# Kernel optimization log

Hardware: AMD Instinct MI355X
Metric: run time of the kernel (lower is better)

The kernel has to match this reference:

```python
import jax, jax.numpy as jnp
import numpy as np

B, N, DIM, H, DH = 2, 2048, 512, 8, 64
EPS = 1e-3  # eps added after relu feature map, per original


def setup_inputs() -> dict:
    key = jax.random.key(0)
    k0, k1, k2, k3, k4 = jax.random.split(key, 5)
    s_in = 1.0 / np.sqrt(DIM)
    s_out = 1.0 / np.sqrt(H * DH)
    return {
        "x": jax.random.normal(k0, (B, N, DIM), jnp.float32),
        "Wq": jax.random.normal(k1, (DIM, H * DH), jnp.float32) * s_in,
        "Wk": jax.random.normal(k2, (DIM, H * DH), jnp.float32) * s_in,
        "Wv": jax.random.normal(k3, (DIM, H * DH), jnp.float32) * s_in,
        "Wo": jax.random.normal(k4, (H * DH, DIM), jnp.float32) * s_out,
        "bo": jnp.zeros((DIM,), jnp.float32),
    }


def causal_linear_attn(q, k, v, eps=EPS):
    # bucket_size == 1 path of the original causal_linear_attn (blindspot_size=1):
    # relu feature map + eps, running cumsums of k and of the outer product k v^T.
    q = jax.nn.relu(q) + eps
    k = jax.nn.relu(k) + eps
    k_cum = jnp.cumsum(k, axis=2)                                  # [b,h,n,d]
    ctx = jnp.cumsum(k[..., :, None] * v[..., None, :], axis=2)    # [b,h,n,d,e]
    d_inv = 1.0 / jnp.einsum('bhnd,bhnd->bhn', q, k_cum)           # [b,h,n]
    return jnp.einsum('bhnd,bhnde,bhn->bhne', q, ctx, d_inv)       # [b,h,n,e]


def reference(x, Wq, Wk, Wv, Wo, bo):
    b, n, _ = x.shape
    split = lambda t: t.reshape(b, n, H, DH).transpose(0, 2, 1, 3)  # [b,h,n,dh]
    q = split(x @ Wq)
    k = split(x @ Wk)
    v = split(x @ Wv)
    out = causal_linear_attn(q, k, v)
    out = out.transpose(0, 2, 1, 3).reshape(b, n, H * DH)
    return out @ Wo + bo
```

## Files before the change

### kernel.cpp

```cpp
#include <hip/hip_runtime.h>

constexpr int kB   = 2;
constexpr int kN   = 2048;
constexpr int kDIM = 512;
constexpr int kH   = 8;
constexpr int kDH  = 64;
constexpr int kBH  = kB * kH;
constexpr int NROWS = kB * kN;
constexpr int CHUNK = 64;
constexpr int NCH   = kN / CHUNK;
constexpr int CBSTRIDE = kDH * kDH + kDH;
constexpr float kEPS = 1e-3f;

typedef _Float16 f16x8 __attribute__((ext_vector_type(8)));
typedef _Float16 f16x4 __attribute__((ext_vector_type(4)));
typedef float    floatx4 __attribute__((ext_vector_type(4)));

__device__ __forceinline__ void async_copy16(void* lds, const void* g) {
    __builtin_amdgcn_global_load_lds(
        (const __attribute__((address_space(1))) void*)g,
        (__attribute__((address_space(3))) void*)lds,
        16, 0, 0);
}

__global__ __launch_bounds__(256)
void convert_x_kernel(const float* __restrict__ x, _Float16* __restrict__ xh)
{
    const int i = blockIdx.x * 256 + threadIdx.x;
    const float4 a = *(const float4*)(x + (size_t)i * 8);
    const float4 b = *(const float4*)(x + (size_t)i * 8 + 4);
    f16x8 o;
    o[0] = (_Float16)a.x; o[1] = (_Float16)a.y; o[2] = (_Float16)a.z; o[3] = (_Float16)a.w;
    o[4] = (_Float16)b.x; o[5] = (_Float16)b.y; o[6] = (_Float16)b.z; o[7] = (_Float16)b.w;
    *(f16x8*)(xh + (size_t)i * 8) = o;
}

__global__ __launch_bounds__(256)
void convert_wT_kernel(const float* __restrict__ Wq, const float* __restrict__ Wk,
                       const float* __restrict__ Wv, const float* __restrict__ Wo,
                       _Float16* __restrict__ WT, _Float16* __restrict__ WoT)
{
    __shared__ float tile[32][33];
    const int z = blockIdx.z;
    const float* src = (z == 0) ? Wq : (z == 1) ? Wk : (z == 2) ? Wv : Wo;
    _Float16* dst = (z < 3) ? (WT + (size_t)z * 512 * 512) : WoT;
    const int r0 = blockIdx.y * 32, c0 = blockIdx.x * 32;
    const int tr = threadIdx.x >> 5, tc = threadIdx.x & 31;
    #pragma unroll
    for (int i = 0; i < 4; ++i)
        tile[tr + 8 * i][tc] = src[(size_t)(r0 + tr + 8 * i) * 512 + c0 + tc];
    __syncthreads();
    #pragma unroll
    for (int i = 0; i < 4; ++i)
        dst[(size_t)(c0 + tr + 8 * i) * 512 + r0 + tc] = (_Float16)tile[tc][tr + 8 * i];
}

template<int MODE>
__global__ __launch_bounds__(256)
void mfma_gemm_kernel(const _Float16* __restrict__ A,
                      const _Float16* __restrict__ BT,
                      const float* __restrict__ bo,
                      float* __restrict__ o0,
                      float* __restrict__ o1,
                      float* __restrict__ o2)
{
    constexpr int BM = 128, BN = 128, BK = 64, K = 512;
    __shared__ _Float16 As[BM * BK];
    __shared__ _Float16 Bs[BN * BK];

    const int t = threadIdx.x;
    const int l = t & 63;
    const int w = t >> 6;
    const int wm = w >> 1, wn = w & 1;
    const int m0 = blockIdx.x * BM;
    const int n0 = blockIdx.y * BN;

    const int r15 = l & 15, kq = l >> 4, sw = r15 & 7;

    floatx4 acc[4][4];
    #pragma unroll
    for (int mi = 0; mi < 4; ++mi)
        #pragma unroll
        for (int ni = 0; ni < 4; ++ni)
            acc[mi][ni] = (floatx4){0.f, 0.f, 0.f, 0.f};

    const int srow  = t >> 3;
    const int sslot = t & 7;

    const char* Abase = (const char*)(A + (size_t)m0 * K);
    const char* Bbase = (const char*)(BT + (size_t)n0 * K);
    char* AsB = (char*)As;
    char* BsB = (char*)Bs;

    const char* ArdB = (const char*)As + (wm * 64 + r15) * 128;
    const char* BrdB = (const char*)Bs + (wn * 64 + r15) * 128;
    const int sw0 = ((kq ^ sw) << 4);
    const int sw1 = (((4 + kq) ^ sw) << 4);

    for (int k0 = 0; k0 < K; k0 += BK) {
        #pragma unroll
        for (int i = 0; i < 4; ++i) {
            const int row = i * 32 + srow;
            const int gsl = sslot ^ (row & 7);
            async_copy16(AsB + row * 128 + sslot * 16,
                         Abase + (size_t)row * (K * 2) + k0 * 2 + gsl * 16);
            async_copy16(BsB + row * 128 + sslot * 16,
                         Bbase + (size_t)row * (K * 2) + k0 * 2 + gsl * 16);
        }
        __syncthreads();

        f16x8 af[4][2], bf[4][2];
        #pragma unroll
        for (int i = 0; i < 4; ++i) {
            af[i][0] = *(const f16x8*)(ArdB + i * 2048 + sw0);
            af[i][1] = *(const f16x8*)(ArdB + i * 2048 + sw1);
            bf[i][0] = *(const f16x8*)(BrdB + i * 2048 + sw0);
            bf[i][1] = *(const f16x8*)(BrdB + i * 2048 + sw1);
        }
        #pragma unroll
        for (int kh = 0; kh < 2; ++kh)
            #pragma unroll
            for (int mi = 0; mi < 4; ++mi)
                #pragma unroll
                for (int ni = 0; ni < 4; ++ni)
                    acc[mi][ni] = __builtin_amdgcn_mfma_f32_16x16x32_f16(
                        af[mi][kh], bf[ni][kh], acc[mi][ni], 0, 0, 0);
        __syncthreads();
    }

    if (MODE == 0) {
        const int which = n0 >> 9;
        float* dst = (which == 0) ? o0 : (which == 1) ? o1 : o2;
        #pragma unroll
        for (int ni = 0; ni < 4; ++ni) {
            const int col = n0 + wn * 64 + ni * 16 + r15;
            const int h = (col >> 6) & 7, e = col & 63;
            #pragma unroll
            for (int mi = 0; mi < 4; ++mi) {
                #pragma unroll
                for (int r = 0; r < 4; ++r) {
                    const int row = m0 + wm * 64 + mi * 16 + kq * 4 + r;
                    const int b = row >> 11, n = row & 2047;
                    float v = acc[mi][ni][r];
                    if (which < 2) v = fmaxf(v, 0.f) + kEPS;
                    dst[((size_t)((b << 3) + h) * 2048 + n) * 64 + e] = v;
                }
            }
        }
    } else {
        #pragma unroll
        for (int ni = 0; ni < 4; ++ni) {
            const int col = n0 + wn * 64 + ni * 16 + r15;
            const float bias = bo[col];
            #pragma unroll
            for (int mi = 0; mi < 4; ++mi) {
                const int row = m0 + wm * 64 + mi * 16 + kq * 4;
                #pragma unroll
                for (int r = 0; r < 4; ++r)
                    o0[(size_t)(row + r) * 512 + col] = acc[mi][ni][r] + bias;
            }
        }
    }
}

__global__ __launch_bounds__(256)
void chunk_sum_kernel(const float* __restrict__ kb, const float* __restrict__ vb,
                      float* __restrict__ cbuf)
{
    const int ch = blockIdx.x, bh = blockIdx.y;
    const int t = threadIdx.x;
    const int tx = t & 15, ty = t >> 4;

    __shared__ float ks[64][65];
    __shared__ float vs[64][68];

    const float* kp = kb + ((size_t)bh * kN + (size_t)ch * CHUNK) * kDH;
    const float* vp = vb + ((size_t)bh * kN + (size_t)ch * CHUNK) * kDH;

    #pragma unroll
    for (int it = 0; it < 4; ++it) {
        int idx = it * 1024 + t * 4;
        int row = idx >> 6, col = idx & 63;
        float4 k4 = *(const float4*)(kp + (size_t)row * kDH + col);
        ks[row][col + 0] = k4.x; ks[row][col + 1] = k4.y;
        ks[row][col + 2] = k4.z; ks[row][col + 3] = k4.w;
        float4 v4 = *(const float4*)(vp + (size_t)row * kDH + col);
        vs[row][col + 0] = v4.x; vs[row][col + 1] = v4.y;
        vs[row][col + 2] = v4.z; vs[row][col + 3] = v4.w;
    }
    __syncthreads();

    float acc[4][4] = {};
    for (int n = 0; n < 64; ++n) {
        float kr[4], vr[4];
        #pragma unroll
        for (int i = 0; i < 4; ++i) kr[i] = ks[n][ty * 4 + i];
        #pragma unroll
        for (int j = 0; j < 4; ++j) vr[j] = vs[n][tx * 4 + j];
        #pragma unroll
        for (int i = 0; i < 4; ++i)
            #pragma unroll
            for (int j = 0; j < 4; ++j)
                acc[i][j] += kr[i] * vr[j];
    }

    float* out = cbuf + ((size_t)bh * NCH + ch) * CBSTRIDE;
    #pragma unroll
    for (int i = 0; i < 4; ++i) {
        float4 o; o.x = acc[i][0]; o.y = acc[i][1]; o.z = acc[i][2]; o.w = acc[i][3];
        *(float4*)(out + (size_t)(ty * 4 + i) * kDH + tx * 4) = o;
    }
    if (t < 64) {
        float z = 0.f;
        for (int n = 0; n < 64; ++n) z += ks[n][t];
        out[kDH * kDH + t] = z;
    }
}

__global__ __launch_bounds__(256)
void prefix_kernel(float* __restrict__ cbuf)
{
    const int bh = blockIdx.y;
    const int i = blockIdx.x * 256 + threadIdx.x;
    if (i >= CBSTRIDE) return;
    float* base = cbuf + (size_t)bh * NCH * CBSTRIDE + i;
    float vals[NCH];
    #pragma unroll
    for (int c = 0; c < NCH; ++c) vals[c] = base[(size_t)c * CBSTRIDE];
    float acc = 0.f;
    #pragma unroll
    for (int c = 0; c < NCH; ++c) {
        float tmp = vals[c];
        base[(size_t)c * CBSTRIDE] = acc;
        acc += tmp;
    }
}

__global__ __launch_bounds__(256)
void chunk_out_kernel(const float* __restrict__ qb, const float* __restrict__ kb,
                      const float* __restrict__ vb, const float* __restrict__ cbuf,
                      _Float16* __restrict__ attnh)
{
    const int ch = blockIdx.x, bh = blockIdx.y;
    const int t = threadIdx.x;
    const int tx = t & 15, ty = t >> 4;

    __shared__ float qs[64][65];
    __shared__ float kvs[64][68];
    __shared__ float asA[64][65];
    __shared__ float denp[64][17];
    __shared__ float denf[64];

    const float* qp = qb + ((size_t)bh * kN + (size_t)ch * CHUNK) * kDH;
    const float* kp = kb + ((size_t)bh * kN + (size_t)ch * CHUNK) * kDH;
    const float* vp = vb + ((size_t)bh * kN + (size_t)ch * CHUNK) * kDH;
    const float* spre = cbuf + ((size_t)bh * NCH + ch) * CBSTRIDE;

    #pragma unroll
    for (int it = 0; it < 4; ++it) {
        int idx = it * 1024 + t * 4;
        int row = idx >> 6, col = idx & 63;
        float4 q4 = *(const float4*)(qp + (size_t)row * kDH + col);
        qs[row][col + 0] = q4.x; qs[row][col + 1] = q4.y;
        qs[row][col + 2] = q4.z; qs[row][col + 3] = q4.w;
        float4 k4 = *(const float4*)(kp + (size_t)row * kDH + col);
        kvs[row][col + 0] = k4.x; kvs[row][col + 1] = k4.y;
        kvs[row][col + 2] = k4.z; kvs[row][col + 3] = k4.w;
    }
    __syncthreads();

    float acc[4][4] = {};
    for (int d = 0; d < 64; ++d) {
        float qr[4], kr[4];
        #pragma unroll
        for (int i = 0; i < 4; ++i) qr[i] = qs[ty * 4 + i][d];
        #pragma unroll
        for (int j = 0; j < 4; ++j) kr[j] = kvs[tx * 4 + j][d];
        #pragma unroll
        for (int i = 0; i < 4; ++i)
            #pragma unroll
            for (int j = 0; j < 4; ++j)
                acc[i][j] += qr[i] * kr[j];
    }
    __syncthreads();

    #pragma unroll
    for (int i = 0; i < 4; ++i) {
        float p = 0.f;
        #pragma unroll
        for (int j = 0; j < 4; ++j) {
            float a = (tx * 4 + j <= ty * 4 + i) ? acc[i][j] : 0.f;
            asA[ty * 4 + i][tx * 4 + j] = a;
            p += a;
        }
        denp[ty * 4 + i][tx] = p;
    }
    #pragma unroll
    for (int it = 0; it < 4; ++it) {
        int idx = it * 1024 + t * 4;
        int row = idx >> 6, col = idx & 63;
        float4 v4 = *(const float4*)(vp + (size_t)row * kDH + col);
        kvs[row][col + 0] = v4.x; kvs[row][col + 1] = v4.y;
        kvs[row][col + 2] = v4.z; kvs[row][col + 3] = v4.w;
    }
    __syncthreads();

    if (t < 64) {
        float dsum = 0.f;
        #pragma unroll
        for (int x2 = 0; x2 < 16; ++x2) dsum += denp[t][x2];
        const float* z = spre + kDH * kDH;
        for (int d = 0; d < 64; ++d) dsum += qs[t][d] * z[d];
        denf[t] = 1.0f / dsum;
    }

    float o[4][4] = {};
    for (int m = 0; m < 64; ++m) {
        float ar[4], vr[4];
        #pragma unroll
        for (int i = 0; i < 4; ++i) ar[i] = asA[ty * 4 + i][m];
        #pragma unroll
        for (int j = 0; j < 4; ++j) vr[j] = kvs[m][tx * 4 + j];
        #pragma unroll
        for (int i = 0; i < 4; ++i)
            #pragma unroll
            for (int j = 0; j < 4; ++j)
                o[i][j] += ar[i] * vr[j];
    }
    for (int d = 0; d < 64; ++d) {
        float qr[4];
        #pragma unroll
        for (int i = 0; i < 4; ++i) qr[i] = qs[ty * 4 + i][d];
        const float4 s4 = *(const float4*)(spre + (size_t)d * kDH + tx * 4);
        #pragma unroll
        for (int i = 0; i < 4; ++i) {
            o[i][0] += qr[i] * s4.x; o[i][1] += qr[i] * s4.y;
            o[i][2] += qr[i] * s4.z; o[i][3] += qr[i] * s4.w;
        }
    }
    __syncthreads();

    const int b = bh >> 3, h = bh & 7;
    #pragma unroll
    for (int i = 0; i < 4; ++i) {
        int n = ch * CHUNK + ty * 4 + i;
        float di = denf[ty * 4 + i];
        f16x4 st;
        st[0] = (_Float16)(o[i][0] * di);
        st[1] = (_Float16)(o[i][1] * di);
        st[2] = (_Float16)(o[i][2] * di);
        st[3] = (_Float16)(o[i][3] * di);
        *(f16x4*)(attnh + (((size_t)(b * kN + n)) << 9) + h * 64 + tx * 4) = st;
    }
}

extern "C" void kernel_launch(void* const* d_in, const int* in_sizes, int n_in,
                              void* d_out, int out_size, void* d_ws, size_t ws_size,
                              hipStream_t stream)
{
    const float* x  = (const float*)d_in[0];
    const float* Wq = (const float*)d_in[1];
    const float* Wk = (const float*)d_in[2];
    const float* Wv = (const float*)d_in[3];
    const float* Wo = (const float*)d_in[4];
    const float* bo = (const float*)d_in[5];
    float* out = (float*)d_out;

    char* ws = (char*)d_ws;
    float*    qb    = (float*)(ws + 0);
    float*    kb    = (float*)(ws + 8388608);
    float*    vb    = (float*)(ws + 16777216);
    float*    cbuf  = (float*)(ws + 25165824);
    _Float16* xh    = (_Float16*)(ws + 33685504);
    _Float16* WT    = (_Float16*)(ws + 37879808);
    _Float16* WoT   = (_Float16*)(ws + 39452672);
    _Float16* attnh = xh;

    convert_x_kernel<<<1024, 256, 0, stream>>>(x, xh);
    convert_wT_kernel<<<dim3(16, 16, 4), 256, 0, stream>>>(Wq, Wk, Wv, Wo, WT, WoT);
    mfma_gemm_kernel<0><<<dim3(NROWS / 128, 12), 256, 0, stream>>>(xh, WT, nullptr, qb, kb, vb);
    chunk_sum_kernel<<<dim3(NCH, kBH), 256, 0, stream>>>(kb, vb, cbuf);
    prefix_kernel<<<dim3(17, kBH), 256, 0, stream>>>(cbuf);
    chunk_out_kernel<<<dim3(NCH, kBH), 256, 0, stream>>>(qb, kb, vb, cbuf, attnh);
    mfma_gemm_kernel<1><<<dim3(NROWS / 128, 4), 256, 0, stream>>>(attnh, WoT, bo, out, nullptr, nullptr);
}
```

Measured before the change: 68.23 us.

## Move chunked linear-attention math to fp16 MFMA with transposed K/V layouts

The QKV projection now writes q, k and v as fp16, plus transposed copies of k and v, in place of fp32 buffers. The chunk-sum and chunk-output kernels replace scalar FMA loops with 16x16x32 fp16 MFMA instructions, and the prefix scan emits an fp16 copy of the state together with an fp32 normaliser. This should cut memory traffic and scalar ALU work in the attention stages, at the cost of extra transposed writes and reduced precision in the intermediates.

```diff
diff --git a/kernel.cpp b/kernel.cpp
--- a/kernel.cpp
+++ b/kernel.cpp
@@ -60,9 +60,11 @@
 void mfma_gemm_kernel(const _Float16* __restrict__ A,
                       const _Float16* __restrict__ BT,
                       const float* __restrict__ bo,
-                      float* __restrict__ o0,
-                      float* __restrict__ o1,
-                      float* __restrict__ o2)
+                      float* __restrict__ outf,
+                      _Float16* __restrict__ qh,
+                      _Float16* __restrict__ khb,
+                      _Float16* __restrict__ kTh,
+                      _Float16* __restrict__ vTh)
 {
     constexpr int BM = 128, BN = 128, BK = 64, K = 512;
     __shared__ _Float16 As[BM * BK];
@@ -118,32 +120,51 @@
             bf[i][1] = *(const f16x8*)(BrdB + i * 2048 + sw1);
         }
         #pragma unroll
-        for (int kh = 0; kh < 2; ++kh)
+        for (int kk = 0; kk < 2; ++kk)
             #pragma unroll
             for (int mi = 0; mi < 4; ++mi)
                 #pragma unroll
                 for (int ni = 0; ni < 4; ++ni)
                     acc[mi][ni] = __builtin_amdgcn_mfma_f32_16x16x32_f16(
-                        af[mi][kh], bf[ni][kh], acc[mi][ni], 0, 0, 0);
+                        af[mi][kk], bf[ni][kk], acc[mi][ni], 0, 0, 0);
         __syncthreads();
     }
 
     if (MODE == 0) {
-        const int which = n0 >> 9;
-        float* dst = (which == 0) ? o0 : (which == 1) ? o1 : o2;
         #pragma unroll
         for (int ni = 0; ni < 4; ++ni) {
             const int col = n0 + wn * 64 + ni * 16 + r15;
+            const int which = col >> 9;
             const int h = (col >> 6) & 7, e = col & 63;
             #pragma unroll
             for (int mi = 0; mi < 4; ++mi) {
+                const int row0 = m0 + wm * 64 + mi * 16 + kq * 4;
+                const int b = row0 >> 11, nn = row0 & 2047;
+                const int bh = b * 8 + h;
+                float vv[4];
                 #pragma unroll
                 for (int r = 0; r < 4; ++r) {
-                    const int row = m0 + wm * 64 + mi * 16 + kq * 4 + r;
-                    const int b = row >> 11, n = row & 2047;
                     float v = acc[mi][ni][r];
                     if (which < 2) v = fmaxf(v, 0.f) + kEPS;
-                    dst[((size_t)((b << 3) + h) * 2048 + n) * 64 + e] = v;
+                    vv[r] = v;
+                }
+                if (which == 0) {
+                    #pragma unroll
+                    for (int r = 0; r < 4; ++r)
+                        qh[((size_t)bh * kN + nn + r) * 64 + e] = (_Float16)vv[r];
+                } else if (which == 1) {
+                    #pragma unroll
+                    for (int r = 0; r < 4; ++r)
+                        khb[((size_t)bh * kN + nn + r) * 64 + e] = (_Float16)vv[r];
+                    f16x4 t4;
+                    t4[0] = (_Float16)vv[0]; t4[1] = (_Float16)vv[1];
+                    t4[2] = (_Float16)vv[2]; t4[3] = (_Float16)vv[3];
+                    *(f16x4*)(kTh + ((size_t)bh * 64 + e) * kN + nn) = t4;
+                } else {
+                    f16x4 t4;
+                    t4[0] = (_Float16)vv[0]; t4[1] = (_Float16)vv[1];
+                    t4[2] = (_Float16)vv[2]; t4[3] = (_Float16)vv[3];
+                    *(f16x4*)(vTh + ((size_t)bh * 64 + e) * kN + nn) = t4;
                 }
             }
         }
@@ -157,200 +178,197 @@
                 const int row = m0 + wm * 64 + mi * 16 + kq * 4;
                 #pragma unroll
                 for (int r = 0; r < 4; ++r)
-                    o0[(size_t)(row + r) * 512 + col] = acc[mi][ni][r] + bias;
+                    outf[(size_t)(row + r) * 512 + col] = acc[mi][ni][r] + bias;
             }
         }
     }
 }
 
 __global__ __launch_bounds__(256)
-void chunk_sum_kernel(const float* __restrict__ kb, const float* __restrict__ vb,
+void chunk_sum_kernel(const _Float16* __restrict__ kTh, const _Float16* __restrict__ vTh,
                       float* __restrict__ cbuf)
 {
     const int ch = blockIdx.x, bh = blockIdx.y;
-    const int t = threadIdx.x;
-    const int tx = t & 15, ty = t >> 4;
-
-    __shared__ float ks[64][65];
-    __shared__ float vs[64][68];
-
-    const float* kp = kb + ((size_t)bh * kN + (size_t)ch * CHUNK) * kDH;
-    const float* vp = vb + ((size_t)bh * kN + (size_t)ch * CHUNK) * kDH;
-
-    #pragma unroll
-    for (int it = 0; it < 4; ++it) {
-        int idx = it * 1024 + t * 4;
-        int row = idx >> 6, col = idx & 63;
-        float4 k4 = *(const float4*)(kp + (size_t)row * kDH + col);
-        ks[row][col + 0] = k4.x; ks[row][col + 1] = k4.y;
-        ks[row][col + 2] = k4.z; ks[row][col + 3] = k4.w;
-        float4 v4 = *(const float4*)(vp + (size_t)row * kDH + col);
-        vs[row][col + 0] = v4.x; vs[row][col + 1] = v4.y;
-        vs[row][col + 2] = v4.z; vs[row][col + 3] = v4.w;
-    }
-    __syncthreads();
-
-    float acc[4][4] = {};
-    for (int n = 0; n < 64; ++n) {
-        float kr[4], vr[4];
-        #pragma unroll
-        for (int i = 0; i < 4; ++i) kr[i] = ks[n][ty * 4 + i];
-        #pragma unroll
-        for (int j = 0; j < 4; ++j) vr[j] = vs[n][tx * 4 + j];
-        #pragma unroll
-        for (int i = 0; i < 4; ++i)
+    const int t = threadIdx.x, l = t & 63, w = t >> 6;
+    const int r15 = l & 15, kq = l >> 4;
+
+    const _Float16* vbase = vTh + (size_t)bh * 64 * kN + ch * 64;
+    const _Float16* kbase = kTh + (size_t)bh * 64 * kN + ch * 64;
+
+    f16x8 av[2], bk[4][2];
+    #pragma unroll
+    for (int kk = 0; kk < 2; ++kk) {
+        av[kk] = *(const f16x8*)(vbase + (size_t)(w * 16 + r15) * kN + kk * 32 + kq * 8);
+        #pragma unroll
+        for (int ni = 0; ni < 4; ++ni)
+            bk[ni][kk] = *(const f16x8*)(kbase + (size_t)(ni * 16 + r15) * kN + kk * 32 + kq * 8);
+    }
+    floatx4 acc[4];
+    #pragma unroll
+    for (int ni = 0; ni < 4; ++ni) acc[ni] = (floatx4){0.f, 0.f, 0.f, 0.f};
+    #pragma unroll
+    for (int kk = 0; kk < 2; ++kk)
+        #pragma unroll
+        for (int ni = 0; ni < 4; ++ni)
+            acc[ni] = __builtin_amdgcn_mfma_f32_16x16x32_f16(av[kk], bk[ni][kk], acc[ni], 0, 0, 0);
+
+    float* out = cbuf + ((size_t)bh * NCH + ch) * CBSTRIDE;
+    #pragma unroll
+    for (int ni = 0; ni < 4; ++ni)
+        #pragma unroll
+        for (int r = 0; r < 4; ++r)
+            out[(size_t)(w * 16 + kq * 4 + r) * 64 + ni * 16 + r15] = acc[ni][r];
+
+    if (t < 64) {
+        const _Float16* kp = kbase + (size_t)t * kN;
+        float z = 0.f;
+        #pragma unroll
+        for (int j = 0; j < 8; ++j) {
+            f16x8 v8 = *(const f16x8*)(kp + j * 8);
             #pragma unroll
-            for (int j = 0; j < 4; ++j)
-                acc[i][j] += kr[i] * vr[j];
-    }
-
-    float* out = cbuf + ((size_t)bh * NCH + ch) * CBSTRIDE;
-    #pragma unroll
-    for (int i = 0; i < 4; ++i) {
-        float4 o; o.x = acc[i][0]; o.y = acc[i][1]; o.z = acc[i][2]; o.w = acc[i][3];
-        *(float4*)(out + (size_t)(ty * 4 + i) * kDH + tx * 4) = o;
-    }
-    if (t < 64) {
-        float z = 0.f;
-        for (int n = 0; n < 64; ++n) z += ks[n][t];
-        out[kDH * kDH + t] = z;
-    }
-}
-
-__global__ __launch_bounds__(256)
-void prefix_kernel(float* __restrict__ cbuf)
+            for (int u = 0; u < 8; ++u) z += (float)v8[u];
+        }
+        out[4096 + t] = z;
+    }
+}
+
+__global__ __launch_bounds__(256)
+void prefix_kernel(const float* __restrict__ cbuf, _Float16* __restrict__ spre16,
+                   float* __restrict__ zpre)
 {
     const int bh = blockIdx.y;
     const int i = blockIdx.x * 256 + threadIdx.x;
     if (i >= CBSTRIDE) return;
-    float* base = cbuf + (size_t)bh * NCH * CBSTRIDE + i;
+    const float* src = cbuf + (size_t)bh * NCH * CBSTRIDE + i;
+    _Float16* dst = spre16 + (size_t)bh * NCH * CBSTRIDE + i;
+    float* zp = zpre + (size_t)bh * NCH * 64;
+    const bool isz = (i >= 4096);
     float vals[NCH];
     #pragma unroll
-    for (int c = 0; c < NCH; ++c) vals[c] = base[(size_t)c * CBSTRIDE];
-    float acc = 0.f;
+    for (int c = 0; c < NCH; ++c) vals[c] = src[(size_t)c * CBSTRIDE];
+    float a = 0.f;
     #pragma unroll
     for (int c = 0; c < NCH; ++c) {
-        float tmp = vals[c];
-        base[(size_t)c * CBSTRIDE] = acc;
-        acc += tmp;
-    }
-}
-
-__global__ __launch_bounds__(256)
-void chunk_out_kernel(const float* __restrict__ qb, const float* __restrict__ kb,
-                      const float* __restrict__ vb, const float* __restrict__ cbuf,
-                      _Float16* __restrict__ attnh)
+        dst[(size_t)c * CBSTRIDE] = (_Float16)a;
+        if (isz) zp[c * 64 + (i - 4096)] = a;
+        a += vals[c];
+    }
+}
+
+__global__ __launch_bounds__(256)
+void chunk_out_kernel(const _Float16* __restrict__ qh, const _Float16* __restrict__ khb,
+                      const _Float16* __restrict__ vTh, const _Float16* __restrict__ spre16,
+                      const float* __restrict__ zpre, _Float16* __restrict__ attnh)
 {
     const int ch = blockIdx.x, bh = blockIdx.y;
-    const int t = threadIdx.x;
-    const int tx = t & 15, ty = t >> 4;
-
-    __shared__ float qs[64][65];
-    __shared__ float kvs[64][68];
-    __shared__ float asA[64][65];
-    __shared__ float denp[64][17];
+    const int t = threadIdx.x, l = t & 63, w = t >> 6;
+    const int r15 = l & 15, kq = l >> 4;
+
+    __shared__ _Float16 Plds[64 * 64];
+    __shared__ float denp[64];
     __shared__ float denf[64];
 
-    const float* qp = qb + ((size_t)bh * kN + (size_t)ch * CHUNK) * kDH;
-    const float* kp = kb + ((size_t)bh * kN + (size_t)ch * CHUNK) * kDH;
-    const float* vp = vb + ((size_t)bh * kN + (size_t)ch * CHUNK) * kDH;
-    const float* spre = cbuf + ((size_t)bh * NCH + ch) * CBSTRIDE;
-
-    #pragma unroll
-    for (int it = 0; it < 4; ++it) {
-        int idx = it * 1024 + t * 4;
-        int row = idx >> 6, col = idx & 63;
-        float4 q4 = *(const float4*)(qp + (size_t)row * kDH + col);
-        qs[row][col + 0] = q4.x; qs[row][col + 1] = q4.y;
-        qs[row][col + 2] = q4.z; qs[row][col + 3] = q4.w;
-        float4 k4 = *(const float4*)(kp + (size_t)row * kDH + col);
-        kvs[row][col + 0] = k4.x; kvs[row][col + 1] = k4.y;
-        kvs[row][col + 2] = k4.z; kvs[row][col + 3] = k4.w;
+    const size_t rowbase = (size_t)bh * kN + ch * 64;
+
+    f16x8 aq[2], bk[4][2];
+    #pragma unroll
+    for (int kk = 0; kk < 2; ++kk) {
+        aq[kk] = *(const f16x8*)(qh + (rowbase + w * 16 + r15) * 64 + kk * 32 + kq * 8);
+        #pragma unroll
+        for (int ni = 0; ni < 4; ++ni)
+            bk[ni][kk] = *(const f16x8*)(khb + (rowbase + ni * 16 + r15) * 64 + kk * 32 + kq * 8);
+    }
+    floatx4 sacc[4];
+    #pragma unroll
+    for (int ni = 0; ni < 4; ++ni) sacc[ni] = (floatx4){0.f, 0.f, 0.f, 0.f};
+    #pragma unroll
+    for (int kk = 0; kk < 2; ++kk)
+        #pragma unroll
+        for (int ni = 0; ni < 4; ++ni)
+            sacc[ni] = __builtin_amdgcn_mfma_f32_16x16x32_f16(aq[kk], bk[ni][kk], sacc[ni], 0, 0, 0);
+
+    const int qrow = w * 16 + kq * 4;
+    float psum[4] = {0.f, 0.f, 0.f, 0.f};
+    #pragma unroll
+    for (int ni = 0; ni < 4; ++ni) {
+        const int m = ni * 16 + r15;
+        #pragma unroll
+        for (int r = 0; r < 4; ++r) {
+            const int row = qrow + r;
+            const float v = (m <= row) ? sacc[ni][r] : 0.f;
+            psum[r] += v;
+            const int byte = row * 128 + ((((unsigned)m >> 3) ^ (row & 7)) << 4) + (m & 7) * 2;
+            *(_Float16*)((char*)Plds + byte) = (_Float16)v;
+        }
+    }
+    #pragma unroll
+    for (int r = 0; r < 4; ++r) {
+        float p = psum[r];
+        p += __shfl_xor(p, 1, 16);
+        p += __shfl_xor(p, 2, 16);
+        p += __shfl_xor(p, 4, 16);
+        p += __shfl_xor(p, 8, 16);
+        if (r15 == 0) denp[qrow + r] = p;
     }
     __syncthreads();
 
-    float acc[4][4] = {};
-    for (int d = 0; d < 64; ++d) {
-        float qr[4], kr[4];
-        #pragma unroll
-        for (int i = 0; i < 4; ++i) qr[i] = qs[ty * 4 + i][d];
-        #pragma unroll
-        for (int j = 0; j < 4; ++j) kr[j] = kvs[tx * 4 + j][d];
-        #pragma unroll
-        for (int i = 0; i < 4; ++i)
+    if (t < 64) {
+        const _Float16* qp = qh + (rowbase + t) * 64;
+        const float* zp = zpre + ((size_t)bh * NCH + ch) * 64;
+        float s = denp[t];
+        #pragma unroll
+        for (int j = 0; j < 8; ++j) {
+            f16x8 q8 = *(const f16x8*)(qp + j * 8);
             #pragma unroll
-            for (int j = 0; j < 4; ++j)
-                acc[i][j] += qr[i] * kr[j];
-    }
+            for (int u = 0; u < 8; ++u) s += (float)q8[u] * zp[j * 8 + u];
+        }
+        denf[t] = 1.0f / s;
+    }
+
+    f16x8 ap[2], bv[4][2], bs[4][2];
+    #pragma unroll
+    for (int km = 0; km < 2; ++km)
+        ap[km] = *(const f16x8*)((char*)Plds + (w * 16 + r15) * 128 +
+                                 (((km * 4 + kq) ^ (r15 & 7)) << 4));
+    #pragma unroll
+    for (int ni = 0; ni < 4; ++ni) {
+        #pragma unroll
+        for (int km = 0; km < 2; ++km)
+            bv[ni][km] = *(const f16x8*)(vTh + ((size_t)bh * 64 + ni * 16 + r15) * kN +
+                                         ch * 64 + km * 32 + kq * 8);
+    }
+    const _Float16* sp = spre16 + ((size_t)bh * NCH + ch) * CBSTRIDE;
+    #pragma unroll
+    for (int ni = 0; ni < 4; ++ni)
+        #pragma unroll
+        for (int kd = 0; kd < 2; ++kd)
+            bs[ni][kd] = *(const f16x8*)(sp + (size_t)(ni * 16 + r15) * 64 + kd * 32 + kq * 8);
+
+    floatx4 oacc[4];
+    #pragma unroll
+    for (int ni = 0; ni < 4; ++ni) oacc[ni] = (floatx4){0.f, 0.f, 0.f, 0.f};
+    #pragma unroll
+    for (int km = 0; km < 2; ++km)
+        #pragma unroll
+        for (int ni = 0; ni < 4; ++ni)
+            oacc[ni] = __builtin_amdgcn_mfma_f32_16x16x32_f16(ap[km], bv[ni][km], oacc[ni], 0, 0, 0);
+    #pragma unroll
+    for (int kd = 0; kd < 2; ++kd)
+        #pragma unroll
+        for (int ni = 0; ni < 4; ++ni)
+            oacc[ni] = __builtin_amdgcn_mfma_f32_16x16x32_f16(aq[kd], bs[ni][kd], oacc[ni], 0, 0, 0);
     __syncthreads();
 
-    #pragma unroll
-    for (int i = 0; i < 4; ++i) {
-        float p = 0.f;
-        #pragma unroll
-        for (int j = 0; j < 4; ++j) {
-            float a = (tx * 4 + j <= ty * 4 + i) ? acc[i][j] : 0.f;
-            asA[ty * 4 + i][tx * 4 + j] = a;
-            p += a;
-        }
-        denp[ty * 4 + i][tx] = p;
-    }
-    #pragma unroll
-    for (int it = 0; it < 4; ++it) {
-        int idx = it * 1024 + t * 4;
-        int row = idx >> 6, col = idx & 63;
-        float4 v4 = *(const float4*)(vp + (size_t)row * kDH + col);
-        kvs[row][col + 0] = v4.x; kvs[row][col + 1] = v4.y;
-        kvs[row][col + 2] = v4.z; kvs[row][col + 3] = v4.w;
-    }
-    __syncthreads();
-
-    if (t < 64) {
-        float dsum = 0.f;
-        #pragma unroll
-        for (int x2 = 0; x2 < 16; ++x2) dsum += denp[t][x2];
-        const float* z = spre + kDH * kDH;
-        for (int d = 0; d < 64; ++d) dsum += qs[t][d] * z[d];
-        denf[t] = 1.0f / dsum;
-    }
-
-    float o[4][4] = {};
-    for (int m = 0; m < 64; ++m) {
-        float ar[4], vr[4];
-        #pragma unroll
-        for (int i = 0; i < 4; ++i) ar[i] = asA[ty * 4 + i][m];
-        #pragma unroll
-        for (int j = 0; j < 4; ++j) vr[j] = kvs[m][tx * 4 + j];
-        #pragma unroll
-        for (int i = 0; i < 4; ++i)
-            #pragma unroll
-            for (int j = 0; j < 4; ++j)
-                o[i][j] += ar[i] * vr[j];
-    }
-    for (int d = 0; d < 64; ++d) {
-        float qr[4];
-        #pragma unroll
-        for (int i = 0; i < 4; ++i) qr[i] = qs[ty * 4 + i][d];
-        const float4 s4 = *(const float4*)(spre + (size_t)d * kDH + tx * 4);
-        #pragma unroll
-        for (int i = 0; i < 4; ++i) {
-            o[i][0] += qr[i] * s4.x; o[i][1] += qr[i] * s4.y;
-            o[i][2] += qr[i] * s4.z; o[i][3] += qr[i] * s4.w;
-        }
-    }
-    __syncthreads();
-
     const int b = bh >> 3, h = bh & 7;
     #pragma unroll
-    for (int i = 0; i < 4; ++i) {
-        int n = ch * CHUNK + ty * 4 + i;
-        float di = denf[ty * 4 + i];
-        f16x4 st;
-        st[0] = (_Float16)(o[i][0] * di);
-        st[1] = (_Float16)(o[i][1] * di);
-        st[2] = (_Float16)(o[i][2] * di);
-        st[3] = (_Float16)(o[i][3] * di);
-        *(f16x4*)(attnh + (((size_t)(b * kN + n)) << 9) + h * 64 + tx * 4) = st;
+    for (int ni = 0; ni < 4; ++ni) {
+        const int e = ni * 16 + r15;
+        #pragma unroll
+        for (int r = 0; r < 4; ++r) {
+            const int qn = qrow + r;
+            const float ov = oacc[ni][r] * denf[qn];
+            attnh[((size_t)(b * kN + ch * 64 + qn)) * 512 + h * 64 + e] = (_Float16)ov;
+        }
     }
 }
 
@@ -367,20 +385,25 @@
     float* out = (float*)d_out;
 
     char* ws = (char*)d_ws;
-    float*    qb    = (float*)(ws + 0);
-    float*    kb    = (float*)(ws + 8388608);
-    float*    vb    = (float*)(ws + 16777216);
-    float*    cbuf  = (float*)(ws + 25165824);
-    _Float16* xh    = (_Float16*)(ws + 33685504);
-    _Float16* WT    = (_Float16*)(ws + 37879808);
-    _Float16* WoT   = (_Float16*)(ws + 39452672);
-    _Float16* attnh = xh;
+    _Float16* qh     = (_Float16*)(ws + 0);
+    _Float16* khb    = (_Float16*)(ws + 4194304);
+    _Float16* kTh    = (_Float16*)(ws + 8388608);
+    _Float16* vTh    = (_Float16*)(ws + 12582912);
+    float*    cbuf   = (float*)(ws + 16777216);
+    _Float16* spre16 = (_Float16*)(ws + 25296896);
+    float*    zpre   = (float*)(ws + 29556736);
+    _Float16* xh     = (_Float16*)(ws + 29687808);
+    _Float16* WT     = (_Float16*)(ws + 33882112);
+    _Float16* WoT    = (_Float16*)(ws + 35454976);
+    _Float16* attnh  = xh;
 
     convert_x_kernel<<<1024, 256, 0, stream>>>(x, xh);
     convert_wT_kernel<<<dim3(16, 16, 4), 256, 0, stream>>>(Wq, Wk, Wv, Wo, WT, WoT);
-    mfma_gemm_kernel<0><<<dim3(NROWS / 128, 12), 256, 0, stream>>>(xh, WT, nullptr, qb, kb, vb);
-    chunk_sum_kernel<<<dim3(NCH, kBH), 256, 0, stream>>>(kb, vb, cbuf);
-    prefix_kernel<<<dim3(17, kBH), 256, 0, stream>>>(cbuf);
-    chunk_out_kernel<<<dim3(NCH, kBH), 256, 0, stream>>>(qb, kb, vb, cbuf, attnh);
-    mfma_gemm_kernel<1><<<dim3(NROWS / 128, 4), 256, 0, stream>>>(attnh, WoT, bo, out, nullptr, nullptr);
-}
+    mfma_gemm_kernel<0><<<dim3(NROWS / 128, 12), 256, 0, stream>>>(
+        xh, WT, nullptr, nullptr, qh, khb, kTh, vTh);
+    chunk_sum_kernel<<<dim3(NCH, kBH), 256, 0, stream>>>(kTh, vTh, cbuf);
+    prefix_kernel<<<dim3(17, kBH), 256, 0, stream>>>(cbuf, spre16, zpre);
+    chunk_out_kernel<<<dim3(NCH, kBH), 256, 0, stream>>>(qh, khb, vTh, spre16, zpre, attnh);
+    mfma_gemm_kernel<1><<<dim3(NROWS / 128, 4), 256, 0, stream>>>(
+        attnh, WoT, bo, out, nullptr, nullptr, nullptr, nullptr);
+}
```

Result: faster. 56.48 us (-17.2%).
